# Performance work log

Hardware: AMD Instinct MI355X
Metric: run time of the kernel (lower is better)

## Reference

```python
import jax, jax.numpy as jnp
import numpy as np

N_NODES = 100000
N_EDGES = 3200000
NODE_DIM = 16      # output_size_node
EDGE_IN = 2 * NODE_DIM  # input_size_Edge = 32
EDGE_OUT = 9
HIDDEN = 9
MSG_ROUNDS = 3


def _mlp_params(key, d_in, d_hid, d_out):
    k1, k2, k3 = jax.random.split(key, 3)
    s1 = 1.0 / np.sqrt(d_in)
    s2 = 1.0 / np.sqrt(d_hid)
    return (
        jax.random.normal(k1, (d_in, d_hid), jnp.float32) * s1,
        jnp.zeros((d_hid,), jnp.float32),
        jax.random.normal(k2, (d_hid, d_hid), jnp.float32) * s2,
        jnp.zeros((d_hid,), jnp.float32),
        jax.random.normal(k3, (d_hid, d_out), jnp.float32) * s2,
        jnp.zeros((d_out,), jnp.float32),
    )


def setup_inputs() -> dict:
    key = jax.random.key(0)
    kx, ks, kd, kfe, kfx = jax.random.split(key, 5)
    X = jax.random.normal(kx, (N_NODES, NODE_DIM), jnp.float32)
    edge_src = jax.random.randint(ks, (N_EDGES,), 0, N_NODES, jnp.int32)
    edge_dst = jax.random.randint(kd, (N_EDGES,), 0, N_NODES, jnp.int32)
    fe = _mlp_params(kfe, EDGE_IN, HIDDEN, EDGE_OUT)
    fx = _mlp_params(kfx, EDGE_OUT + NODE_DIM, HIDDEN, NODE_DIM)
    return {
        "X": X, "edge_src": edge_src, "edge_dst": edge_dst,
        "fe_W1": fe[0], "fe_b1": fe[1], "fe_W2": fe[2], "fe_b2": fe[3], "fe_W3": fe[4], "fe_b3": fe[5],
        "fx_W1": fx[0], "fx_b1": fx[1], "fx_W2": fx[2], "fx_b2": fx[3], "fx_W3": fx[4], "fx_b3": fx[5],
    }


def _mlp3(h, W1, b1, W2, b2, W3, b3):
    # 3-layer MLP with relu hidden activations (MLP_nonlinear, act='relu')
    h = jax.nn.relu(h @ W1 + b1)
    h = jax.nn.relu(h @ W2 + b2)
    return h @ W3 + b3


def reference(X, edge_src, edge_dst,
              fe_W1, fe_b1, fe_W2, fe_b2, fe_W3, fe_b3,
              fx_W1, fx_b1, fx_W2, fx_b2, fx_W3, fx_b3):
    n = X.shape[0]
    for _ in range(MSG_ROUNDS):
        # per-edge message: fe(cat(X[i], X[j])) with i=receiver(dst), j=sender(src)
        e_in = jnp.concatenate([X[edge_dst], X[edge_src]], axis=-1)  # [E, 2*D]
        msgs = _mlp3(e_in, fe_W1, fe_b1, fe_W2, fe_b2, fe_W3, fe_b3)  # [E, 9]
        m = jax.ops.segment_sum(msgs, edge_dst, num_segments=n)       # [N, 9]
        # per-node update: fx(cat(X[i], m_i))
        X = _mlp3(jnp.concatenate([X, m], axis=-1),
                  fx_W1, fx_b1, fx_W2, fx_b2, fx_W3, fx_b3)           # [N, D]
    return X
```

## Files before the change

kernel.cpp:

```cpp
#include <hip/hip_runtime.h>


constexpr int NN = 100000;
constexpr int NE = 3200000;
constexpr int NBK = (NN + 127) / 128;
constexpr int SLOT = 8192;
constexpr int EPB = 4096;
constexpr int NBLK_SORT = (NE + EPB - 1) / EPB;
constexpr int NB_NODE = (NN + 255) / 256;


__global__ __launch_bounds__(256) void init_k(int* __restrict__ gcursor)
{
    int i = blockIdx.x * 256 + threadIdx.x;
    if (i < NBK) gcursor[i] = i * SLOT;
}


__global__ __launch_bounds__(256) void bsort_k(const int* __restrict__ src,
                                               const int* __restrict__ dst,
                                               int* __restrict__ gcursor,
                                               unsigned* __restrict__ sed)
{
    __shared__ int lhist[NBK];
    __shared__ int lbase[NBK];
    const int t = threadIdx.x;
    for (int i = t; i < NBK; i += 256) lhist[i] = 0;
    __syncthreads();

    const int blkbase = blockIdx.x * EPB;
    unsigned pr[16], sv[16];
    #pragma unroll
    for (int k = 0; k < 16; ++k) {
        const int e = blkbase + k * 256 + t;
        if (e < NE) {
            const int d = dst[e];
            const int s = src[e];
            const int bin = d >> 7;
            const int r = atomicAdd(&lhist[bin], 1);
            pr[k] = ((unsigned)bin << 13) | (unsigned)r;
            sv[k] = ((unsigned)(d & 127) << 17) | (unsigned)s;
        } else {
            pr[k] = 0xFFFFFFFFu;
        }
    }
    __syncthreads();

    for (int i = t; i < NBK; i += 256) {
        const int c = lhist[i];
        if (c) lbase[i] = atomicAdd(&gcursor[i], c);
    }
    __syncthreads();

    #pragma unroll
    for (int k = 0; k < 16; ++k) {
        if (pr[k] != 0xFFFFFFFFu) {
            const int bin = (int)(pr[k] >> 13);
            const int r = (int)(pr[k] & 0x1FFFu);
            sed[lbase[bin] + r] = sv[k];
        }
    }
}


__global__ __launch_bounds__(512) void lsort_k(unsigned* __restrict__ sed,
                                               const int* __restrict__ gcursor)
{
    __shared__ unsigned buf[SLOT];
    __shared__ unsigned obuf[SLOT];
    __shared__ int hist[128];
    __shared__ int cur[128];
    const int t = threadIdx.x;
    const int b = blockIdx.x;
    const int base = b * SLOT;
    int fill = gcursor[b] - base;
    if (fill > SLOT) fill = SLOT;

    if (t < 128) hist[t] = 0;
    __syncthreads();
    for (int i = t; i < fill; i += 512) {
        unsigned v = sed[base + i];
        buf[i] = v;
        atomicAdd(&hist[v >> 17], 1);
    }
    __syncthreads();
    if (t < 128) cur[t] = hist[t];
    __syncthreads();
    for (int off = 1; off < 128; off <<= 1) {
        int a = (t < 128 && t >= off) ? cur[t - off] : 0;
        __syncthreads();
        if (t < 128) cur[t] += a;
        __syncthreads();
    }
    if (t < 128) cur[t] -= hist[t];
    __syncthreads();
    for (int i = t; i < fill; i += 512) {
        unsigned v = buf[i];
        int r = atomicAdd(&cur[v >> 17], 1);
        obuf[r] = v;
    }
    __syncthreads();
    for (int i = t; i < fill; i += 512) sed[base + i] = obuf[i];
}


__global__ __launch_bounds__(256) void base_k(const float* __restrict__ X,
                                              const float* __restrict__ feW1,
                                              const float* __restrict__ feb1,
                                              float* __restrict__ base1,
                                              float* __restrict__ bases,
                                              float* __restrict__ m)
{
    __shared__ float sW[32 * 12], sb[9];
    const int t = threadIdx.x;
    for (int i = t; i < 288; i += 256) sW[(i / 9) * 12 + (i % 9)] = feW1[i];
    if (t < 9) sb[t] = feb1[t];
    __syncthreads();

    const int n = blockIdx.x * 256 + t;
    if (n >= NN) return;

    float x[16];
    const float4* p = reinterpret_cast<const float4*>(X + (size_t)n * 16);
    #pragma unroll
    for (int q = 0; q < 4; ++q) {
        float4 v = p[q];
        x[4*q] = v.x; x[4*q+1] = v.y; x[4*q+2] = v.z; x[4*q+3] = v.w;
    }
    float bd[9];
    #pragma unroll
    for (int j = 0; j < 9; ++j) bd[j] = sb[j];
    #pragma unroll
    for (int i = 0; i < 16; ++i) {
        const float xi = x[i];
        #pragma unroll
        for (int j = 0; j < 9; ++j) bd[j] = fmaf(xi, sW[i * 12 + j], bd[j]);
    }
    float bs[9];
    #pragma unroll
    for (int j = 0; j < 9; ++j) bs[j] = 0.f;
    #pragma unroll
    for (int i = 0; i < 16; ++i) {
        const float xi = x[i];
        #pragma unroll
        for (int j = 0; j < 9; ++j) bs[j] = fmaf(xi, sW[(16 + i) * 12 + j], bs[j]);
    }
    float* bp = base1 + (size_t)n * 12;
    #pragma unroll
    for (int j = 0; j < 9; ++j) bp[j] = bd[j];
    float* sp = bases + (size_t)n * 16;
    #pragma unroll
    for (int j = 0; j < 9; ++j) sp[j] = bs[j];
    float* mp = m + (size_t)n * 9;
    #pragma unroll
    for (int j = 0; j < 9; ++j) mp[j] = 0.f;
}


__global__ __launch_bounds__(256) void edge5_k(
    const float* __restrict__ base1,
    const float* __restrict__ bases,
    const unsigned* __restrict__ sed,
    const int* __restrict__ gcursor,
    const float* __restrict__ feW2, const float* __restrict__ feb2,
    const float* __restrict__ feW3, const float* __restrict__ feb3,
    float* __restrict__ m)
{
    const int t = threadIdx.x;
    const int b = blockIdx.x >> 5;
    const int idx0 = (blockIdx.x & 31) * 256;
    const int fill = gcursor[b] - b * SLOT;
    if (idx0 >= fill) return;

    __shared__ float sW2[9 * 12], sW3[9 * 12], sb2[9], sb3[9];
    if (t < 81)  sW2[(t / 9) * 12 + (t % 9)] = feW2[t];
    if (t >= 128 && t < 209) { int i = t - 128; sW3[(i / 9) * 12 + (i % 9)] = feW3[i]; }
    if (t >= 224 && t < 233) sb2[t - 224] = feb2[t - 224];
    if (t >= 240 && t < 249) sb3[t - 240] = feb3[t - 240];
    __syncthreads();

    const int idx = idx0 + t;
    const bool valid = idx < fill;
    const int lane = t & 63;
    if (__ballot(valid) == 0ull) return;

    int dl;
    float o[9];
    if (valid) {
        const unsigned pk = sed[b * SLOT + idx];
        dl = (int)(pk >> 17);
        const int s = (int)(pk & 0x1FFFFu);

        float a[9];
        {
            const float4* pb = reinterpret_cast<const float4*>(base1 + (size_t)(b * 128 + dl) * 12);
            float4 b0 = pb[0], b1 = pb[1];
            const float b8 = base1[(size_t)(b * 128 + dl) * 12 + 8];
            const float4* ps = reinterpret_cast<const float4*>(bases + (size_t)s * 16);
            float4 c0 = ps[0], c1 = ps[1];
            const float c8 = bases[(size_t)s * 16 + 8];
            a[0] = b0.x + c0.x; a[1] = b0.y + c0.y; a[2] = b0.z + c0.z; a[3] = b0.w + c0.w;
            a[4] = b1.x + c1.x; a[5] = b1.y + c1.y; a[6] = b1.z + c1.z; a[7] = b1.w + c1.w;
            a[8] = b8 + c8;
        }
        #pragma unroll
        for (int j = 0; j < 9; ++j) a[j] = fmaxf(a[j], 0.f);

        float h2[9];
        #pragma unroll
        for (int j = 0; j < 9; ++j) h2[j] = sb2[j];
        #pragma unroll
        for (int i = 0; i < 9; ++i) {
            const float ai = a[i];
            #pragma unroll
            for (int j = 0; j < 9; ++j) h2[j] = fmaf(ai, sW2[i * 12 + j], h2[j]);
        }
        #pragma unroll
        for (int j = 0; j < 9; ++j) h2[j] = fmaxf(h2[j], 0.f);

        #pragma unroll
        for (int j = 0; j < 9; ++j) o[j] = sb3[j];
        #pragma unroll
        for (int i = 0; i < 9; ++i) {
            const float hi = h2[i];
            #pragma unroll
            for (int j = 0; j < 9; ++j) o[j] = fmaf(hi, sW3[i * 12 + j], o[j]);
        }
    } else {
        dl = 128 + lane;
        #pragma unroll
        for (int j = 0; j < 9; ++j) o[j] = 0.f;
    }

    const int dprev = __shfl_up(dl, 1);
    const bool head = (lane == 0) || (dprev != dl);
    const unsigned long long hm = __ballot(head);
    const int dist = __clzll((long long)(hm << (63 - lane)));
    #pragma unroll
    for (int off = 1; off < 64; off <<= 1) {
        const bool ok = (dist >= off);
        #pragma unroll
        for (int j = 0; j < 9; ++j) {
            const float ov = __shfl_up(o[j], off);
            o[j] += ok ? ov : 0.f;
        }
    }
    const bool tail = (lane == 63) || (((hm >> (lane + 1)) & 1ull) != 0ull);
    if (tail && valid) {
        float* mp = m + (size_t)(b * 128 + dl) * 9;
        #pragma unroll
        for (int j = 0; j < 9; ++j) atomicAdd(mp + j, o[j]);
    }
}


__global__ __launch_bounds__(256) void node4_k(
    const float* __restrict__ Xin, float* __restrict__ m,
    const float* __restrict__ fxW1, const float* __restrict__ fxb1,
    const float* __restrict__ fxW2, const float* __restrict__ fxb2,
    const float* __restrict__ fxW3, const float* __restrict__ fxb3,
    const float* __restrict__ feW1, const float* __restrict__ feb1,
    float* __restrict__ Xout, float* __restrict__ base1out,
    float* __restrict__ basesout)
{
    __shared__ float sU1[25 * 12], sU2[9 * 12], sU3[9 * 16];
    __shared__ float sW1d[16 * 12], sW1s[16 * 12];
    __shared__ float sNB[34], sEB1[9];
    const int t = threadIdx.x;
    if (t < 225) sU1[(t / 9) * 12 + (t % 9)] = fxW1[t];
    if (t < 81)  sU2[(t / 9) * 12 + (t % 9)] = fxW2[t];
    if (t < 144) sU3[t] = fxW3[t];
    if (t < 144) sW1d[(t / 9) * 12 + (t % 9)] = feW1[t];
    if (t >= 112) { int i = t - 112; sW1s[(i / 9) * 12 + (i % 9)] = feW1[144 + i]; }
    if (t < 9) sNB[t] = fxb1[t];
    if (t >= 32 && t < 41) sNB[9 + (t - 32)] = fxb2[t - 32];
    if (t >= 64 && t < 80) sNB[18 + (t - 64)] = fxb3[t - 64];
    if (t >= 96 && t < 105) sEB1[t - 96] = feb1[t - 96];
    __syncthreads();

    const int n = blockIdx.x * 256 + t;
    if (n >= NN) return;

    float xr[16];
    {
        const float4* p = reinterpret_cast<const float4*>(Xin + (size_t)n * 16);
        #pragma unroll
        for (int q = 0; q < 4; ++q) {
            float4 v = p[q];
            xr[4*q] = v.x; xr[4*q+1] = v.y; xr[4*q+2] = v.z; xr[4*q+3] = v.w;
        }
    }
    float mm[9];
    float* mp = m + (size_t)n * 9;
    #pragma unroll
    for (int j = 0; j < 9; ++j) mm[j] = mp[j];
    #pragma unroll
    for (int j = 0; j < 9; ++j) mp[j] = 0.f;

    float h1[9];
    #pragma unroll
    for (int j = 0; j < 9; ++j) h1[j] = sNB[j];
    #pragma unroll
    for (int i = 0; i < 16; ++i) {
        const float xi = xr[i];
        #pragma unroll
        for (int j = 0; j < 9; ++j) h1[j] = fmaf(xi, sU1[i * 12 + j], h1[j]);
    }
    #pragma unroll
    for (int i = 0; i < 9; ++i) {
        const float xi = mm[i];
        #pragma unroll
        for (int j = 0; j < 9; ++j) h1[j] = fmaf(xi, sU1[(16 + i) * 12 + j], h1[j]);
    }
    #pragma unroll
    for (int j = 0; j < 9; ++j) h1[j] = fmaxf(h1[j], 0.f);

    float h2[9];
    #pragma unroll
    for (int j = 0; j < 9; ++j) h2[j] = sNB[9 + j];
    #pragma unroll
    for (int i = 0; i < 9; ++i) {
        const float xi = h1[i];
        #pragma unroll
        for (int j = 0; j < 9; ++j) h2[j] = fmaf(xi, sU2[i * 12 + j], h2[j]);
    }
    #pragma unroll
    for (int j = 0; j < 9; ++j) h2[j] = fmaxf(h2[j], 0.f);

    float o[16];
    #pragma unroll
    for (int k = 0; k < 16; ++k) o[k] = sNB[18 + k];
    #pragma unroll
    for (int j = 0; j < 9; ++j) {
        const float hj = h2[j];
        #pragma unroll
        for (int k = 0; k < 16; ++k) o[k] = fmaf(hj, sU3[j * 16 + k], o[k]);
    }

    float4* po = reinterpret_cast<float4*>(Xout + (size_t)n * 16);
    #pragma unroll
    for (int q = 0; q < 4; ++q) {
        float4 v;
        v.x = o[4*q]; v.y = o[4*q+1]; v.z = o[4*q+2]; v.w = o[4*q+3];
        po[q] = v;
    }

    float bb[9];
    #pragma unroll
    for (int j = 0; j < 9; ++j) bb[j] = sEB1[j];
    #pragma unroll
    for (int i = 0; i < 16; ++i) {
        const float xi = o[i];
        #pragma unroll
        for (int j = 0; j < 9; ++j) bb[j] = fmaf(xi, sW1d[i * 12 + j], bb[j]);
    }
    float* bp = base1out + (size_t)n * 12;
    #pragma unroll
    for (int j = 0; j < 9; ++j) bp[j] = bb[j];

    float cc[9];
    #pragma unroll
    for (int j = 0; j < 9; ++j) cc[j] = 0.f;
    #pragma unroll
    for (int i = 0; i < 16; ++i) {
        const float xi = o[i];
        #pragma unroll
        for (int j = 0; j < 9; ++j) cc[j] = fmaf(xi, sW1s[i * 12 + j], cc[j]);
    }
    float* sp = basesout + (size_t)n * 16;
    #pragma unroll
    for (int j = 0; j < 9; ++j) sp[j] = cc[j];
}

extern "C" void kernel_launch(void* const* d_in, const int* in_sizes, int n_in,
                              void* d_out, int out_size, void* d_ws, size_t ws_size,
                              hipStream_t stream)
{
    (void)in_sizes; (void)n_in; (void)out_size; (void)ws_size;
    const float* X0   = (const float*)d_in[0];
    const int*   esrc = (const int*)d_in[1];
    const int*   edst = (const int*)d_in[2];
    const float* feW1 = (const float*)d_in[3];
    const float* feb1 = (const float*)d_in[4];
    const float* feW2 = (const float*)d_in[5];
    const float* feb2 = (const float*)d_in[6];
    const float* feW3 = (const float*)d_in[7];
    const float* feb3 = (const float*)d_in[8];
    const float* fxW1 = (const float*)d_in[9];
    const float* fxb1 = (const float*)d_in[10];
    const float* fxW2 = (const float*)d_in[11];
    const float* fxb2 = (const float*)d_in[12];
    const float* fxW3 = (const float*)d_in[13];
    const float* fxb3 = (const float*)d_in[14];
    float* out = (float*)d_out;

    float* base1  = (float*)d_ws;
    float* bases  = base1 + (size_t)NN * 12;
    float* mb     = bases + (size_t)NN * 16;
    int* gcursor  = (int*)(mb + (size_t)NN * 9);
    unsigned* sed = (unsigned*)(gcursor + 1024);

    const dim3 thr(256);
    const dim3 gS(NBLK_SORT);
    const dim3 gL(NBK);
    const dim3 gE(NBK * (SLOT / 256));
    const dim3 gN(NB_NODE);

    init_k<<<4, thr, 0, stream>>>(gcursor);
    bsort_k<<<gS, thr, 0, stream>>>(esrc, edst, gcursor, sed);
    lsort_k<<<gL, dim3(512), 0, stream>>>(sed, gcursor);

    base_k<<<gN, thr, 0, stream>>>(X0, feW1, feb1, base1, bases, mb);
    edge5_k<<<gE, thr, 0, stream>>>(base1, bases, sed, gcursor,
                                    feW2, feb2, feW3, feb3, mb);
    node4_k<<<gN, thr, 0, stream>>>(X0, mb, fxW1, fxb1, fxW2, fxb2, fxW3, fxb3,
                                    feW1, feb1, out, base1, bases);
    edge5_k<<<gE, thr, 0, stream>>>(base1, bases, sed, gcursor,
                                    feW2, feb2, feW3, feb3, mb);
    node4_k<<<gN, thr, 0, stream>>>(out, mb, fxW1, fxb1, fxW2, fxb2, fxW3, fxb3,
                                    feW1, feb1, out, base1, bases);
    edge5_k<<<gE, thr, 0, stream>>>(base1, bases, sed, gcursor,
                                    feW2, feb2, feW3, feb3, mb);
    node4_k<<<gN, thr, 0, stream>>>(out, mb, fxW1, fxb1, fxW2, fxb2, fxW3, fxb3,
                                    feW1, feb1, out, base1, bases);
}
```

Before: 559.1 us.

## Defer final edge MLP layer past segment sum using linearity and degree count

The last linear layer of the edge MLP (W3, b3) is moved out of the per-edge kernel. Edges now accumulate the ReLU hidden activations plus a degree count into a 10-wide buffer, and the node kernel applies W3 and degree*b3 once per node. This removes 81 FMAs per edge in exchange for one extra atomic per segment and a slightly wider accumulator. The cursor init kernel is also replaced by a memset, with offsets made relative to each slot.

Result: no change. 554.7 us (-0.8%).

```diff
diff --git a/kernel.cpp b/kernel.cpp
--- a/kernel.cpp
+++ b/kernel.cpp
@@ -8,13 +8,6 @@
 constexpr int EPB = 4096;
 constexpr int NBLK_SORT = (NE + EPB - 1) / EPB;
 constexpr int NB_NODE = (NN + 255) / 256;
-
-
-__global__ __launch_bounds__(256) void init_k(int* __restrict__ gcursor)
-{
-    int i = blockIdx.x * 256 + threadIdx.x;
-    if (i < NBK) gcursor[i] = i * SLOT;
-}
 
 
 __global__ __launch_bounds__(256) void bsort_k(const int* __restrict__ src,
@@ -57,7 +50,7 @@
         if (pr[k] != 0xFFFFFFFFu) {
             const int bin = (int)(pr[k] >> 13);
             const int r = (int)(pr[k] & 0x1FFFu);
-            sed[lbase[bin] + r] = sv[k];
+            sed[(size_t)bin * SLOT + lbase[bin] + r] = sv[k];
         }
     }
 }
@@ -73,7 +66,7 @@
     const int t = threadIdx.x;
     const int b = blockIdx.x;
     const int base = b * SLOT;
-    int fill = gcursor[b] - base;
+    int fill = gcursor[b];
     if (fill > SLOT) fill = SLOT;
 
     if (t < 128) hist[t] = 0;
@@ -151,32 +144,29 @@
     float* sp = bases + (size_t)n * 16;
     #pragma unroll
     for (int j = 0; j < 9; ++j) sp[j] = bs[j];
-    float* mp = m + (size_t)n * 9;
-    #pragma unroll
-    for (int j = 0; j < 9; ++j) mp[j] = 0.f;
-}
-
-
-__global__ __launch_bounds__(256) void edge5_k(
+    float* mp = m + (size_t)n * 10;
+    #pragma unroll
+    for (int j = 0; j < 10; ++j) mp[j] = 0.f;
+}
+
+
+__global__ __launch_bounds__(256) void edge8_k(
     const float* __restrict__ base1,
     const float* __restrict__ bases,
     const unsigned* __restrict__ sed,
     const int* __restrict__ gcursor,
     const float* __restrict__ feW2, const float* __restrict__ feb2,
-    const float* __restrict__ feW3, const float* __restrict__ feb3,
     float* __restrict__ m)
 {
     const int t = threadIdx.x;
     const int b = blockIdx.x >> 5;
     const int idx0 = (blockIdx.x & 31) * 256;
-    const int fill = gcursor[b] - b * SLOT;
+    const int fill = gcursor[b];
     if (idx0 >= fill) return;
 
-    __shared__ float sW2[9 * 12], sW3[9 * 12], sb2[9], sb3[9];
+    __shared__ float sW2[9 * 12], sb2[9];
     if (t < 81)  sW2[(t / 9) * 12 + (t % 9)] = feW2[t];
-    if (t >= 128 && t < 209) { int i = t - 128; sW3[(i / 9) * 12 + (i % 9)] = feW3[i]; }
-    if (t >= 224 && t < 233) sb2[t - 224] = feb2[t - 224];
-    if (t >= 240 && t < 249) sb3[t - 240] = feb3[t - 240];
+    if (t >= 96 && t < 105) sb2[t - 96] = feb2[t - 96];
     __syncthreads();
 
     const int idx = idx0 + t;
@@ -187,7 +177,7 @@
     int dl;
     float o[9];
     if (valid) {
-        const unsigned pk = sed[b * SLOT + idx];
+        const unsigned pk = sed[(size_t)b * SLOT + idx];
         dl = (int)(pk >> 17);
         const int s = (int)(pk & 0x1FFFFu);
 
@@ -206,26 +196,16 @@
         #pragma unroll
         for (int j = 0; j < 9; ++j) a[j] = fmaxf(a[j], 0.f);
 
-        float h2[9];
-        #pragma unroll
-        for (int j = 0; j < 9; ++j) h2[j] = sb2[j];
+        #pragma unroll
+        for (int j = 0; j < 9; ++j) o[j] = sb2[j];
         #pragma unroll
         for (int i = 0; i < 9; ++i) {
             const float ai = a[i];
             #pragma unroll
-            for (int j = 0; j < 9; ++j) h2[j] = fmaf(ai, sW2[i * 12 + j], h2[j]);
-        }
-        #pragma unroll
-        for (int j = 0; j < 9; ++j) h2[j] = fmaxf(h2[j], 0.f);
-
-        #pragma unroll
-        for (int j = 0; j < 9; ++j) o[j] = sb3[j];
-        #pragma unroll
-        for (int i = 0; i < 9; ++i) {
-            const float hi = h2[i];
-            #pragma unroll
-            for (int j = 0; j < 9; ++j) o[j] = fmaf(hi, sW3[i * 12 + j], o[j]);
-        }
+            for (int j = 0; j < 9; ++j) o[j] = fmaf(ai, sW2[i * 12 + j], o[j]);
+        }
+        #pragma unroll
+        for (int j = 0; j < 9; ++j) o[j] = fmaxf(o[j], 0.f);
     } else {
         dl = 128 + lane;
         #pragma unroll
@@ -247,35 +227,39 @@
     }
     const bool tail = (lane == 63) || (((hm >> (lane + 1)) & 1ull) != 0ull);
     if (tail && valid) {
-        float* mp = m + (size_t)(b * 128 + dl) * 9;
+        float* mp = m + (size_t)(b * 128 + dl) * 10;
         #pragma unroll
         for (int j = 0; j < 9; ++j) atomicAdd(mp + j, o[j]);
-    }
-}
-
-
-__global__ __launch_bounds__(256) void node4_k(
+        atomicAdd(mp + 9, (float)(dist + 1));
+    }
+}
+
+
+__global__ __launch_bounds__(256) void node7_k(
     const float* __restrict__ Xin, float* __restrict__ m,
     const float* __restrict__ fxW1, const float* __restrict__ fxb1,
     const float* __restrict__ fxW2, const float* __restrict__ fxb2,
     const float* __restrict__ fxW3, const float* __restrict__ fxb3,
     const float* __restrict__ feW1, const float* __restrict__ feb1,
+    const float* __restrict__ feW3, const float* __restrict__ feb3,
     float* __restrict__ Xout, float* __restrict__ base1out,
     float* __restrict__ basesout)
 {
     __shared__ float sU1[25 * 12], sU2[9 * 12], sU3[9 * 16];
-    __shared__ float sW1d[16 * 12], sW1s[16 * 12];
-    __shared__ float sNB[34], sEB1[9];
+    __shared__ float sW1d[16 * 12], sW1s[16 * 12], sW3[9 * 12];
+    __shared__ float sNB[34], sEB1[9], sEB3[9];
     const int t = threadIdx.x;
     if (t < 225) sU1[(t / 9) * 12 + (t % 9)] = fxW1[t];
     if (t < 81)  sU2[(t / 9) * 12 + (t % 9)] = fxW2[t];
     if (t < 144) sU3[t] = fxW3[t];
     if (t < 144) sW1d[(t / 9) * 12 + (t % 9)] = feW1[t];
     if (t >= 112) { int i = t - 112; sW1s[(i / 9) * 12 + (i % 9)] = feW1[144 + i]; }
+    if (t >= 16 && t < 97) { int i = t - 16; sW3[(i / 9) * 12 + (i % 9)] = feW3[i]; }
     if (t < 9) sNB[t] = fxb1[t];
     if (t >= 32 && t < 41) sNB[9 + (t - 32)] = fxb2[t - 32];
     if (t >= 64 && t < 80) sNB[18 + (t - 64)] = fxb3[t - 64];
     if (t >= 96 && t < 105) sEB1[t - 96] = feb1[t - 96];
+    if (t >= 128 && t < 137) sEB3[t - 128] = feb3[t - 128];
     __syncthreads();
 
     const int n = blockIdx.x * 256 + t;
@@ -290,12 +274,23 @@
             xr[4*q] = v.x; xr[4*q+1] = v.y; xr[4*q+2] = v.z; xr[4*q+3] = v.w;
         }
     }
+    float S[9], deg;
+    float* mp = m + (size_t)n * 10;
+    #pragma unroll
+    for (int j = 0; j < 9; ++j) S[j] = mp[j];
+    deg = mp[9];
+    #pragma unroll
+    for (int j = 0; j < 10; ++j) mp[j] = 0.f;
+
     float mm[9];
-    float* mp = m + (size_t)n * 9;
-    #pragma unroll
-    for (int j = 0; j < 9; ++j) mm[j] = mp[j];
-    #pragma unroll
-    for (int j = 0; j < 9; ++j) mp[j] = 0.f;
+    #pragma unroll
+    for (int j = 0; j < 9; ++j) mm[j] = deg * sEB3[j];
+    #pragma unroll
+    for (int i = 0; i < 9; ++i) {
+        const float si = S[i];
+        #pragma unroll
+        for (int j = 0; j < 9; ++j) mm[j] = fmaf(si, sW3[i * 12 + j], mm[j]);
+    }
 
     float h1[9];
     #pragma unroll
@@ -397,7 +392,7 @@
     float* base1  = (float*)d_ws;
     float* bases  = base1 + (size_t)NN * 12;
     float* mb     = bases + (size_t)NN * 16;
-    int* gcursor  = (int*)(mb + (size_t)NN * 9);
+    int* gcursor  = (int*)(mb + (size_t)NN * 10);
     unsigned* sed = (unsigned*)(gcursor + 1024);
 
     const dim3 thr(256);
@@ -406,21 +401,18 @@
     const dim3 gE(NBK * (SLOT / 256));
     const dim3 gN(NB_NODE);
 
-    init_k<<<4, thr, 0, stream>>>(gcursor);
+    hipMemsetAsync(gcursor, 0, NBK * sizeof(int), stream);
     bsort_k<<<gS, thr, 0, stream>>>(esrc, edst, gcursor, sed);
     lsort_k<<<gL, dim3(512), 0, stream>>>(sed, gcursor);
 
     base_k<<<gN, thr, 0, stream>>>(X0, feW1, feb1, base1, bases, mb);
-    edge5_k<<<gE, thr, 0, stream>>>(base1, bases, sed, gcursor,
-                                    feW2, feb2, feW3, feb3, mb);
-    node4_k<<<gN, thr, 0, stream>>>(X0, mb, fxW1, fxb1, fxW2, fxb2, fxW3, fxb3,
-                                    feW1, feb1, out, base1, bases);
-    edge5_k<<<gE, thr, 0, stream>>>(base1, bases, sed, gcursor,
-                                    feW2, feb2, feW3, feb3, mb);
-    node4_k<<<gN, thr, 0, stream>>>(out, mb, fxW1, fxb1, fxW2, fxb2, fxW3, fxb3,
-                                    feW1, feb1, out, base1, bases);
-    edge5_k<<<gE, thr, 0, stream>>>(base1, bases, sed, gcursor,
-                                    feW2, feb2, feW3, feb3, mb);
-    node4_k<<<gN, thr, 0, stream>>>(out, mb, fxW1, fxb1, fxW2, fxb2, fxW3, fxb3,
-                                    feW1, feb1, out, base1, bases);
-}
+    edge8_k<<<gE, thr, 0, stream>>>(base1, bases, sed, gcursor, feW2, feb2, mb);
+    node7_k<<<gN, thr, 0, stream>>>(X0, mb, fxW1, fxb1, fxW2, fxb2, fxW3, fxb3,
+                                    feW1, feb1, feW3, feb3, out, base1, bases);
+    edge8_k<<<gE, thr, 0, stream>>>(base1, bases, sed, gcursor, feW2, feb2, mb);
+    node7_k<<<gN, thr, 0, stream>>>(out, mb, fxW1, fxb1, fxW2, fxb2, fxW3, fxb3,
+                                    feW1, feb1, feW3, feb3, out, base1, bases);
+    edge8_k<<<gE, thr, 0, stream>>>(base1, bases, sed, gcursor, feW2, feb2, mb);
+    node7_k<<<gN, thr, 0, stream>>>(out, mb, fxW1, fxb1, fxW2, fxb2, fxW3, fxb3,
+                                    feW1, feb1, feW3, feb3, out, base1, bases);
+}
```
